# Optimization experiments

Measured on AMD Instinct MI355X. Metric: run time of the kernel, lower is better.

Reference implementation:

```python
import jax, jax.numpy as jnp
import numpy as np

H = W = 9
C = 16
D = 34
NHEAD = 2
HDIM = D // NHEAD  # 17
FF = 2048
NLAYERS = 2
EPS = 1e-5


def setup_inputs() -> dict:
    key = jax.random.key(0)
    ks = jax.random.split(key, 16)
    s = 0.05
    return {
        "obs": jax.random.normal(ks[0], (2, H, W), dtype=jnp.float32),
        "conv1_w": jax.random.normal(ks[1], (16, 2, 3, 3), dtype=jnp.float32) * s,
        "conv1_b": jnp.zeros((16,), jnp.float32),
        "conv2_w": jax.random.normal(ks[2], (16, 16, 3, 3), dtype=jnp.float32) * s,
        "conv2_b": jnp.zeros((16,), jnp.float32),
        "in_proj_w": jax.random.normal(ks[3], (NLAYERS, 3 * D, D), dtype=jnp.float32) * s,
        "in_proj_b": jnp.zeros((NLAYERS, 3 * D), jnp.float32),
        "out_proj_w": jax.random.normal(ks[4], (NLAYERS, D, D), dtype=jnp.float32) * s,
        "out_proj_b": jnp.zeros((NLAYERS, D), jnp.float32),
        "lin1_w": jax.random.normal(ks[5], (NLAYERS, FF, D), dtype=jnp.float32) * s,
        "lin1_b": jnp.zeros((NLAYERS, FF), jnp.float32),
        "lin2_w": jax.random.normal(ks[6], (NLAYERS, D, FF), dtype=jnp.float32) * s,
        "lin2_b": jnp.zeros((NLAYERS, D), jnp.float32),
        "ln1_g": jnp.ones((NLAYERS, D), jnp.float32),
        "ln1_b": jnp.zeros((NLAYERS, D), jnp.float32),
        "ln2_g": jnp.ones((NLAYERS, D), jnp.float32),
        "ln2_b": jnp.zeros((NLAYERS, D), jnp.float32),
    }


def _layer_norm(x, g, b):
    m = jnp.mean(x, axis=-1, keepdims=True)
    v = jnp.mean(jnp.square(x - m), axis=-1, keepdims=True)
    return (x - m) * jax.lax.rsqrt(v + EPS) * g + b


def _encoder_layer(x, ipw, ipb, opw, opb, l1w, l1b, l2w, l2b, g1, b1, g2, b2):
    # x: [S, D]. Post-norm TransformerEncoderLayer, eval mode (no dropout).
    S = x.shape[0]
    qkv = x @ ipw.T + ipb  # [S, 3D]
    q, k, v = jnp.split(qkv, 3, axis=-1)
    q = q.reshape(S, NHEAD, HDIM).transpose(1, 0, 2)  # [h, S, d]
    k = k.reshape(S, NHEAD, HDIM).transpose(1, 0, 2)
    v = v.reshape(S, NHEAD, HDIM).transpose(1, 0, 2)
    scores = jnp.einsum("hqd,hkd->hqk", q, k) / jnp.sqrt(jnp.float32(HDIM))
    attn = jax.nn.softmax(scores, axis=-1)
    o = jnp.einsum("hqk,hkd->hqd", attn, v)  # [h, S, d]
    o = o.transpose(1, 0, 2).reshape(S, D)
    o = o @ opw.T + opb
    x = _layer_norm(x + o, g1, b1)
    f = jax.nn.relu(x @ l1w.T + l1b) @ l2w.T + l2b
    return _layer_norm(x + f, g2, b2)


def _conv(x, w, b):
    y = jax.lax.conv_general_dilated(
        x, w, window_strides=(1, 1), padding="SAME",
        dimension_numbers=("NCHW", "OIHW", "NCHW"))
    return jax.nn.relu(y + b[None, :, None, None])


def reference(obs, conv1_w, conv1_b, conv2_w, conv2_b, in_proj_w, in_proj_b,
              out_proj_w, out_proj_b, lin1_w, lin1_b, lin2_w, lin2_b,
              ln1_g, ln1_b, ln2_g, ln2_b):
    x = obs[None]  # [1, 2, H, W]
    x = _conv(x, conv1_w, conv1_b)
    x = _conv(x, conv2_w, conv2_b)
    hw = H * W
    cell_emb = x[0].reshape(C, hw).T  # [hw, C]
    idx = jnp.arange(hw)
    r = (idx // W).astype(jnp.float32)
    c = (idx % W).astype(jnp.float32)
    dx = (r[:, None] - r[None, :]) / ((H - 1) / 2.0)  # [hw, hw]
    dy = (c[:, None] - c[None, :]) / ((W - 1) / 2.0)
    tok_i = jnp.broadcast_to(cell_emb[:, None, :], (hw, hw, C))
    tok_j = jnp.broadcast_to(cell_emb[None, :, :], (hw, hw, C))
    rel = jnp.stack([dx, dy], axis=-1)  # [hw, hw, 2]
    tokens = jnp.concatenate([tok_i, tok_j, rel], axis=-1).reshape(hw * hw, D)
    for l in range(NLAYERS):
        tokens = _encoder_layer(
            tokens, in_proj_w[l], in_proj_b[l], out_proj_w[l], out_proj_b[l],
            lin1_w[l], lin1_b[l], lin2_w[l], lin2_b[l],
            ln1_g[l], ln1_b[l], ln2_g[l], ln2_b[l])
    agent_idx = jnp.argmax(obs[0].reshape(-1))
    start = agent_idx * hw
    agent_tokens = jax.lax.dynamic_slice(tokens, (start, 0), (hw, D))
    return agent_tokens.mean(axis=0)  # [D]
```

## Files before the change

### kernel.cpp

```cpp
#include <hip/hip_runtime.h>
#include <hip/hip_bf16.h>

#define HH 9
#define WW 9
#define HW 81
#define CC 16
#define DD 34
#define SS 6561
#define NHEAD 2
#define HD 17
#define FF 2048
#define EPSF 1e-5f

#define NTILES 52
#define NSPLIT2 26
#define QB 64

#define NIP 7168
#define NOP 3072
#define NW1 131072
#define NW2 98304
#define NLTOT (NIP + NOP + NW1 + NW2)
#define LPREP_BLOCKS 1872
#define NKF 425984
#define NVF 212992
#define NV16 13312
#define ZERO_WORDS 332800
#define ZERO_BLOCKS 1300

typedef __attribute__((ext_vector_type(8))) short bf16x8;
typedef __attribute__((ext_vector_type(4))) float f32x4;

__device__ __forceinline__ unsigned short f2b(float f) {
  unsigned int u = __float_as_uint(f);
  u += 0x7fffu + ((u >> 16) & 1u);
  return (unsigned short)(u >> 16);
}

__global__ __launch_bounds__(256) void prep_kernel(
    const float* __restrict__ obs, const float* __restrict__ w1, const float* __restrict__ b1,
    const float* __restrict__ w2, const float* __restrict__ b2,
    float* __restrict__ cell, int* __restrict__ aidx,
    const float* __restrict__ ipw, const float* __restrict__ opw,
    const float* __restrict__ l1w, const float* __restrict__ l2w,
    unsigned short* __restrict__ ipwp, unsigned short* __restrict__ opwp,
    unsigned short* __restrict__ w1p, unsigned short* __restrict__ w2p,
    unsigned short* __restrict__ kfp, unsigned short* __restrict__ vfp,
    float* __restrict__ v16) {
  int bx = blockIdx.x;
  int t = threadIdx.x;
  if (bx == 0) {
    __shared__ float s_obs[2][11][11];
    __shared__ float s_w1[288];
    __shared__ float s_w2[2304];
    __shared__ float s_b1[16], s_b2[16];
    __shared__ float y1[CC][121];
    for (int i = t; i < 2 * 121; i += 256) ((float*)s_obs)[i] = 0.f;
    for (int i = t; i < CC * 121; i += 256) ((float*)y1)[i] = 0.f;
    for (int i = t; i < 288; i += 256) s_w1[i] = w1[i];
    for (int i = t; i < 2304; i += 256) s_w2[i] = w2[i];
    if (t < 16) { s_b1[t] = b1[t]; s_b2[t] = b2[t]; }
    __syncthreads();
    for (int i = t; i < 2 * HW; i += 256) {
      int ic = i / HW, p = i % HW;
      s_obs[ic][1 + p / WW][1 + p % WW] = obs[i];
    }
    __syncthreads();
    if (t == 0) {
      int best = 0; float bv = s_obs[0][1][1];
      for (int p = 1; p < HW; p++) {
        float v = s_obs[0][1 + p / WW][1 + p % WW];
        if (v > bv) { bv = v; best = p; }
      }
      *aidx = best;
    }
    for (int idx = t; idx < CC * HW; idx += 256) {
      int c = idx / HW, p = idx % HW;
      int i = p / WW, j = p % WW;
      float acc = s_b1[c];
#pragma unroll
      for (int ic = 0; ic < 2; ic++)
#pragma unroll
        for (int di = 0; di < 3; di++)
#pragma unroll
          for (int dj = 0; dj < 3; dj++)
            acc += s_obs[ic][i + di][j + dj] * s_w1[((c * 2 + ic) * 3 + di) * 3 + dj];
      y1[c][(i + 1) * 11 + (j + 1)] = fmaxf(acc, 0.f);
    }
    __syncthreads();
    for (int idx = t; idx < CC * HW; idx += 256) {
      int c = idx / HW, p = idx % HW;
      int i = p / WW, j = p % WW;
      float acc = s_b2[c];
#pragma unroll
      for (int ic = 0; ic < CC; ic++)
#pragma unroll
        for (int di = 0; di < 3; di++)
#pragma unroll
          for (int dj = 0; dj < 3; dj++)
            acc += y1[ic][(i + di) * 11 + (j + dj)] * s_w2[((c * CC + ic) * 3 + di) * 3 + dj];
      cell[p * CC + c] = fmaxf(acc, 0.f);
    }
  } else if (bx <= LPREP_BLOCKS) {
    int i = (bx - 1) * 256 + t;
    int layer = i / NLTOT;
    int r = i % NLTOT;
    if (r < NIP) {
      int n = r >> 6, k = r & 63;
      ipwp[layer * NIP + r] =
          (n < 102 && k < DD) ? f2b(ipw[(size_t)layer * 102 * DD + n * DD + k]) : (unsigned short)0;
    } else if (r < NIP + NOP) {
      int rr = r - NIP;
      int n = rr >> 6, k = rr & 63;
      opwp[layer * NOP + rr] =
          (n < DD && k < DD) ? f2b(opw[(size_t)layer * DD * DD + n * DD + k]) : (unsigned short)0;
    } else if (r < NIP + NOP + NW1) {
      int rr = r - NIP - NOP;
      int f = rr >> 6, k = rr & 63;
      w1p[layer * NW1 + rr] =
          (k < DD) ? f2b(l1w[(size_t)layer * FF * DD + f * DD + k]) : (unsigned short)0;
    } else {
      int rr = r - NIP - NOP - NW1;
      int d = rr >> 11, kk = rr & 2047;
      w2p[layer * NW2 + rr] =
          (d < DD) ? f2b(l2w[(size_t)layer * DD * FF + d * FF + kk]) : (unsigned short)0;
    }
  } else {
    int zi = (bx - 1 - LPREP_BLOCKS) * 256 + t;
    if (zi < NKF / 2) ((unsigned int*)kfp)[zi] = 0u;
    else if (zi < NKF / 2 + NVF / 2) ((unsigned int*)vfp)[zi - NKF / 2] = 0u;
    else if (zi < ZERO_WORDS) v16[zi - NKF / 2 - NVF / 2] = 0.f;
  }
}

__global__ __launch_bounds__(256) void ptprep_kernel(
    const float* __restrict__ cell, const float* __restrict__ ipw,
    const float* __restrict__ ipb, float* __restrict__ Pt) {
  int idx = blockIdx.x * 256 + threadIdx.x;
  if (idx >= 2 * HW * 102) return;
  int part = idx / (HW * 102);
  int rem = idx % (HW * 102);
  int a = rem / 102, n = rem % 102;
  float ra = (float)(a / WW) * 0.25f, ca = (float)(a % WW) * 0.25f;
  float acc;
  if (part == 0) {
    acc = ipb[n] + ipw[n * DD + 32] * ra + ipw[n * DD + 33] * ca;
    for (int f = 0; f < CC; f++) acc += ipw[n * DD + f] * cell[a * CC + f];
  } else {
    acc = -(ipw[n * DD + 32] * ra + ipw[n * DD + 33] * ca);
    for (int f = 0; f < CC; f++) acc += ipw[n * DD + CC + f] * cell[a * CC + f];
  }
  Pt[idx] = acc;
}

__global__ __launch_bounds__(256) void fl1_kernel(
    const float* __restrict__ cell, const float* __restrict__ Pt,
    const unsigned short* __restrict__ opwp, const float* __restrict__ opb,
    const float* __restrict__ g1v, const float* __restrict__ b1v,
    const unsigned short* __restrict__ w1p, const unsigned short* __restrict__ w2p,
    const float* __restrict__ fb1, const float* __restrict__ fb2,
    const float* __restrict__ g2v, const float* __restrict__ b2v,
    float* __restrict__ x) {
  __shared__ float sk[2][2][HW][20];
  __shared__ float sv[2][2][HW][20];
  __shared__ __align__(16) unsigned short soA[16 * 72];
  __shared__ float sxF[16][35];
  __shared__ __align__(16) unsigned short sxA2[16 * 72];
  __shared__ float sxF2[16][35];
  __shared__ __align__(16) unsigned short hw_[4][16 * 40];
  __shared__ float yred[4][16][49];
  int t = threadIdx.x;
  int w = t >> 6, lane = t & 63, quad = lane >> 4, col = lane & 15;
  int r0 = blockIdx.x * 16;
  int nr = min(16, SS - r0);

  for (int i = t; i < 16 * 72; i += 256) { soA[i] = 0; sxA2[i] = 0; }
  for (int i = t; i < 16 * 35; i += 256) { ((float*)sxF)[i] = 0.f; ((float*)sxF2)[i] = 0.f; }
  for (int i = t; i < 2 * 2 * HW * HD; i += 256) {
    int d = i % HD, a = (i / HD) % HW, part = (i / (HD * HW)) & 1, h = i / (HD * HW * 2);
    const float* base = Pt + (size_t)part * HW * 102 + a * 102;
    sk[h][part][a][d] = base[DD + h * HD + d];
    sv[h][part][a][d] = base[2 * DD + h * HD + d];
  }
  for (int i = t; i < nr * DD; i += 256) {
    int r = i / DD, d = i - r * DD;
    int row = r0 + r;
    int ii = row / HW, jj = row - ii * HW;
    float v;
    if (d < CC) v = cell[ii * CC + d];
    else if (d < 2 * CC) v = cell[jj * CC + (d - CC)];
    else if (d == 32) v = (float)((ii / WW) - (jj / WW)) * 0.25f;
    else v = (float)((ii % WW) - (jj % WW)) * 0.25f;
    sxF[r][d] = v;
  }
  __syncthreads();

  {
    int tl = t >> 4, sub = t & 15;
    int h = (sub >> 3) & 1, p = (sub >> 2) & 1, asp = sub & 3;
    int row = r0 + tl;
    int tc = row < SS ? row : SS - 1;
    int ii = tc / HW, jj = tc % HW;
    const float scale = 0.24253562503633297f;
    const float* p0 = Pt + ii * 102 + h * HD;
    const float* p1 = Pt + (size_t)HW * 102 + jj * 102 + h * HD;
    float q[HD];
#pragma unroll
    for (int d = 0; d < HD; d++) q[d] = (p0[d] + p1[d]) * scale;
    float S = 0.f, EV[HD];
#pragma unroll
    for (int d = 0; d < HD; d++) EV[d] = 0.f;
    for (int a = asp; a < HW; a += 4) {
      float s = 0.f;
#pragma unroll
      for (int d = 0; d < HD; d++) s += q[d] * sk[h][p][a][d];
      float e = __expf(fminf(s, 70.f));
      S += e;
#pragma unroll
      for (int d = 0; d < HD; d++) EV[d] += e * sv[h][p][a][d];
    }
    S += __shfl_xor(S, 1); S += __shfl_xor(S, 2);
#pragma unroll
    for (int d = 0; d < HD; d++) { EV[d] += __shfl_xor(EV[d], 1); EV[d] += __shfl_xor(EV[d], 2); }
    float So = __shfl_xor(S, 4);
    float EVo[HD];
#pragma unroll
    for (int d = 0; d < HD; d++) EVo[d] = __shfl_xor(EV[d], 4);
    float inv = 1.f / S, invo = 1.f / So;
    if ((sub & 7) == 0 && tl < nr) {
#pragma unroll
      for (int d = 0; d < HD; d++)
        soA[tl * 72 + h * HD + d] = f2b(EV[d] * inv + EVo[d] * invo);
    }
  }
  __syncthreads();

  if (w == 0) {
    bf16x8 a0 = *(const bf16x8*)&soA[col * 72 + quad * 8];
    bf16x8 a1 = *(const bf16x8*)&soA[col * 72 + 32 + quad * 8];
    f32x4 y[3];
#pragma unroll
    for (int nt = 0; nt < 3; nt++) {
      int n = nt * 16 + col;
      bf16x8 b0 = *(const bf16x8*)&opwp[n * 64 + quad * 8];
      bf16x8 b1 = *(const bf16x8*)&opwp[n * 64 + 32 + quad * 8];
      f32x4 acc = {0.f, 0.f, 0.f, 0.f};
      acc = __builtin_amdgcn_mfma_f32_16x16x32_bf16(a0, b0, acc, 0, 0, 0);
      y[nt] = __builtin_amdgcn_mfma_f32_16x16x32_bf16(a1, b1, acc, 0, 0, 0);
    }
    float yv[3][4];
    float s1[4] = {0.f, 0.f, 0.f, 0.f}, s2[4] = {0.f, 0.f, 0.f, 0.f};
#pragma unroll
    for (int nt = 0; nt < 3; nt++) {
      int d = nt * 16 + col;
      bool vd = d < DD;
      float ob = vd ? opb[d] : 0.f;
#pragma unroll
      for (int r = 0; r < 4; r++) {
        int row = quad * 4 + r;
        float v = vd ? (y[nt][r] + ob + sxF[row][d]) : 0.f;
        yv[nt][r] = v;
        s1[r] += v;
        s2[r] += v * v;
      }
    }
#pragma unroll
    for (int msk = 1; msk <= 8; msk <<= 1)
#pragma unroll
      for (int r = 0; r < 4; r++) {
        s1[r] += __shfl_xor(s1[r], msk);
        s2[r] += __shfl_xor(s2[r], msk);
      }
#pragma unroll
    for (int r = 0; r < 4; r++) {
      int row = quad * 4 + r;
      float mean = s1[r] * (1.f / DD);
      float var = s2[r] * (1.f / DD) - mean * mean;
      float rs = rsqrtf(var + EPSF);
#pragma unroll
      for (int nt = 0; nt < 3; nt++) {
        int d = nt * 16 + col;
        if (d < DD) {
          float o = (yv[nt][r] - mean) * rs * g1v[d] + b1v[d];
          sxF2[row][d] = o;
          sxA2[row * 72 + d] = f2b(o);
        }
      }
    }
  }
  __syncthreads();

  bf16x8 a0 = *(const bf16x8*)&sxA2[col * 72 + quad * 8];
  bf16x8 a1 = *(const bf16x8*)&sxA2[col * 72 + 32 + quad * 8];
  unsigned short* myh = &hw_[w][0];
  f32x4 acc3[3];
#pragma unroll
  for (int nt = 0; nt < 3; nt++) acc3[nt] = (f32x4){0.f, 0.f, 0.f, 0.f};
  for (int kt = 0; kt < 16; kt++) {
    int fbase = kt * 128 + w * 32;
#pragma unroll
    for (int nt = 0; nt < 2; nt++) {
      int f = fbase + nt * 16 + col;
      bf16x8 b0f = *(const bf16x8*)&w1p[f * 64 + quad * 8];
      bf16x8 b1f = *(const bf16x8*)&w1p[f * 64 + 32 + quad * 8];
      f32x4 hacc = {0.f, 0.f, 0.f, 0.f};
      hacc = __builtin_amdgcn_mfma_f32_16x16x32_bf16(a0, b0f, hacc, 0, 0, 0);
      hacc = __builtin_amdgcn_mfma_f32_16x16x32_bf16(a1, b1f, hacc, 0, 0, 0);
      float bias = fb1[f];
#pragma unroll
      for (int r = 0; r < 4; r++) {
        float hv = fmaxf(hacc[r] + bias, 0.f);
        myh[(quad * 4 + r) * 40 + nt * 16 + col] = f2b(hv);
      }
    }
    bf16x8 pa = *(const bf16x8*)&myh[col * 40 + quad * 8];
#pragma unroll
    for (int nt = 0; nt < 3; nt++) {
      int n = nt * 16 + col;
      bf16x8 wb = *(const bf16x8*)&w2p[(size_t)n * FF + fbase + quad * 8];
      acc3[nt] = __builtin_amdgcn_mfma_f32_16x16x32_bf16(pa, wb, acc3[nt], 0, 0, 0);
    }
  }
#pragma unroll
  for (int nt = 0; nt < 3; nt++)
#pragma unroll
    for (int r = 0; r < 4; r++)
      yred[w][quad * 4 + r][nt * 16 + col] = acc3[nt][r];
  __syncthreads();
  if (w == 0) {
    float yv[3][4];
    float s1[4] = {0.f, 0.f, 0.f, 0.f}, s2[4] = {0.f, 0.f, 0.f, 0.f};
#pragma unroll
    for (int nt = 0; nt < 3; nt++) {
      int d = nt * 16 + col;
      bool valid = d < DD;
      float b2x = valid ? fb2[d] : 0.f;
#pragma unroll
      for (int r = 0; r < 4; r++) {
        int row = quad * 4 + r;
        float v = yred[0][row][nt * 16 + col] + yred[1][row][nt * 16 + col]
                + yred[2][row][nt * 16 + col] + yred[3][row][nt * 16 + col];
        v = valid ? (v + b2x + sxF2[row][d]) : 0.f;
        yv[nt][r] = v;
        s1[r] += v;
        s2[r] += v * v;
      }
    }
#pragma unroll
    for (int msk = 1; msk <= 8; msk <<= 1)
#pragma unroll
      for (int r = 0; r < 4; r++) {
        s1[r] += __shfl_xor(s1[r], msk);
        s2[r] += __shfl_xor(s2[r], msk);
      }
#pragma unroll
    for (int r = 0; r < 4; r++) {
      int row = quad * 4 + r;
      if (row >= nr) continue;
      float mean = s1[r] * (1.f / DD);
      float var = s2[r] * (1.f / DD) - mean * mean;
      float rs = rsqrtf(var + EPSF);
#pragma unroll
      for (int nt = 0; nt < 3; nt++) {
        int d = nt * 16 + col;
        if (d < DD)
          x[(size_t)(r0 + row) * DD + d] = (yv[nt][r] - mean) * rs * g2v[d] + b2v[d];
      }
    }
  }
}

__global__ __launch_bounds__(256) void qkv2_kernel(
    const float* __restrict__ x, const unsigned short* __restrict__ ipwp,
    const float* __restrict__ ipb, const int* __restrict__ abase,
    float* __restrict__ qkv, unsigned short* __restrict__ kfp,
    unsigned short* __restrict__ vfp, float* __restrict__ v16) {
  __shared__ __align__(16) unsigned short sxA[32 * 72];
  int t = threadIdx.x;
  int w = t >> 6, lane = t & 63, quad = lane >> 4, col = lane & 15;
  int m0 = (w & 1) * 16, half = w >> 1;
  bool qpart = blockIdx.x >= 206;
  int row0 = qpart ? (abase[0] * HW + (blockIdx.x - 206) * 32) : blockIdx.x * 32;
  int nr = min(32, SS - row0);
  for (int i = t; i < 32 * 72; i += 256) sxA[i] = 0;
  __syncthreads();
  for (int i = t; i < nr * DD; i += 256) {
    int r = i / DD, d = i - r * DD;
    sxA[r * 72 + d] = f2b(x[(size_t)(row0 + r) * DD + d]);
  }
  __syncthreads();
  bf16x8 a0 = *(const bf16x8*)&sxA[(m0 + col) * 72 + quad * 8];
  bf16x8 a1 = *(const bf16x8*)&sxA[(m0 + col) * 72 + 32 + quad * 8];
  if (!qpart) {
    int ntc = half ? 2 : 3;
    for (int nt2 = 0; nt2 < ntc; nt2++) {
      int nt = half * 3 + nt2;
      int n = DD + nt * 16 + col;
      int nc = n < 112 ? n : 111;
      bf16x8 b0 = *(const bf16x8*)&ipwp[nc * 64 + quad * 8];
      bf16x8 b1 = *(const bf16x8*)&ipwp[nc * 64 + 32 + quad * 8];
      f32x4 acc = {0.f, 0.f, 0.f, 0.f};
      acc = __builtin_amdgcn_mfma_f32_16x16x32_bf16(a0, b0, acc, 0, 0, 0);
      acc = __builtin_amdgcn_mfma_f32_16x16x32_bf16(a1, b1, acc, 0, 0, 0);
      if (n < 102) {
        float bias = ipb[n];
        int kd = n - DD;
#pragma unroll
        for (int r = 0; r < 4; r++) {
          int m = m0 + quad * 4 + r;
          if (m >= nr) continue;
          int tok = row0 + m;
          float val = acc[r] + bias;
          int T = tok >> 7, tl = tok & 127;
          if (kd < 2 * HD) {
            int h = kd >= HD;
            int d = kd - h * HD;
            int colf = tl >> 3, ntk = tl & 7;
            kfp[(((size_t)h * NTILES + T) * 8 + ntk) * 512 +
                ((d >> 3) * 16 + colf) * 8 + (d & 7)] = f2b(val);
          } else {
            int vd = kd - 2 * HD;
            int h = vd >= HD;
            int d = vd - h * HD;
            if (d < 16) {
              int c = tl >> 5, qf = (tl >> 3) & 3, j = tl & 7;
              vfp[(((size_t)h * NTILES + T) * 4 + c) * 512 +
                  (qf * 16 + d) * 8 + j] = f2b(val);
            } else {
              v16[(size_t)h * (NTILES * 128) + tok] = val;
            }
          }
        }
      }
    }
  } else {
    int ntc = half ? 1 : 2;
    for (int nt2 = 0; nt2 < ntc; nt2++) {
      int nt = half * 2 + nt2;
      int n = nt * 16 + col;
      bf16x8 b0 = *(const bf16x8*)&ipwp[n * 64 + quad * 8];
      bf16x8 b1 = *(const bf16x8*)&ipwp[n * 64 + 32 + quad * 8];
      f32x4 acc = {0.f, 0.f, 0.f, 0.f};
      acc = __builtin_amdgcn_mfma_f32_16x16x32_bf16(a0, b0, acc, 0, 0, 0);
      acc = __builtin_amdgcn_mfma_f32_16x16x32_bf16(a1, b1, acc, 0, 0, 0);
      if (n < DD) {
        float bias = ipb[n];
#pragma unroll
        for (int r = 0; r < 4; r++) {
          int m = row0 + m0 + quad * 4 + r;
          if (m < SS) qkv[(size_t)m * 102 + n] = acc[r] + bias;
        }
      }
    }
  }
}

__global__ __launch_bounds__(256) void attn2_kernel(
    const float* __restrict__ qkv, const unsigned short* __restrict__ kfp,
    const unsigned short* __restrict__ vfp, const float* __restrict__ v16,
    const int* __restrict__ abase,
    float* __restrict__ opart, float* __restrict__ lpart) {
  __shared__ __align__(16) unsigned short scb[4][16 * 136];
  int t = threadIdx.x, w = t >> 6, lane = t & 63, quad = lane >> 4, col = lane & 15;
  int h = blockIdx.y, sp = blockIdx.z;
  int base = abase[0] * HW;
  int q0 = blockIdx.x * QB;
  const float scale = 0.24253562503633297f;
  const unsigned short* kf = kfp + (size_t)h * (NTILES * 8 * 512);
  const unsigned short* vf = vfp + (size_t)h * (NTILES * 4 * 512);
  const float* v16h = v16 + (size_t)h * (NTILES * 128);
  unsigned short* myscb = &scb[w][0];

  int mq = base + q0 + w * 16 + col;
  int qc = mq < SS ? mq : SS - 1;
  bf16x8 aq;
#pragma unroll
  for (int j = 0; j < 8; j++) {
    int d = quad * 8 + j;
    aq[j] = (short)((d < HD) ? f2b(qkv[(size_t)qc * 102 + h * HD + d] * scale) : 0);
  }

  f32x4 oacc = {0.f, 0.f, 0.f, 0.f};
  float o16a[4] = {0.f, 0.f, 0.f, 0.f};
  float lreg[4] = {0.f, 0.f, 0.f, 0.f};

  for (int tile = sp; tile < NTILES; tile += NSPLIT2) {
    int k0 = tile * 128;
    const unsigned short* kt = kf + (size_t)tile * (8 * 512);
    f32x4 s[8];
#pragma unroll
    for (int nt = 0; nt < 8; nt++) {
      bf16x8 kb = *(const bf16x8*)(kt + nt * 512 + lane * 8);
      f32x4 z = {0.f, 0.f, 0.f, 0.f};
      s[nt] = __builtin_amdgcn_mfma_f32_16x16x32_bf16(aq, kb, z, 0, 0, 0);
    }
    if (k0 + 128 > SS) {
#pragma unroll
      for (int nt = 0; nt < 8; nt++)
        if (k0 + col * 8 + nt >= SS) {
          s[nt][0] = -1e30f; s[nt][1] = -1e30f; s[nt][2] = -1e30f; s[nt][3] = -1e30f;
        }
    }
#pragma unroll
    for (int r = 0; r < 4; r++) {
      bf16x8 pv;
      float psl = 0.f;
#pragma unroll
      for (int nt = 0; nt < 8; nt++) {
        float p = __expf(fminf(s[nt][r], 70.f));
        s[nt][r] = p;
        psl += p;
        pv[nt] = (short)f2b(p);
      }
      lreg[r] += psl;
      *(bf16x8*)(myscb + (quad * 4 + r) * 136 + col * 8) = pv;
    }
    f32x4 va = *(const f32x4*)(v16h + k0 + col * 8);
    f32x4 vb4 = *(const f32x4*)(v16h + k0 + col * 8 + 4);
#pragma unroll
    for (int r = 0; r < 4; r++) {
      o16a[r] += s[0][r] * va[0] + s[1][r] * va[1] + s[2][r] * va[2] + s[3][r] * va[3]
               + s[4][r] * vb4[0] + s[5][r] * vb4[1] + s[6][r] * vb4[2] + s[7][r] * vb4[3];
    }
    const unsigned short* vt = vf + (size_t)tile * (4 * 512);
#pragma unroll
    for (int c = 0; c < 4; c++) {
      bf16x8 pa = *(const bf16x8*)(myscb + col * 136 + c * 32 + quad * 8);
      bf16x8 vbf = *(const bf16x8*)(vt + c * 512 + lane * 8);
      oacc = __builtin_amdgcn_mfma_f32_16x16x32_bf16(pa, vbf, oacc, 0, 0, 0);
    }
  }
#pragma unroll
  for (int msk = 1; msk <= 8; msk <<= 1)
#pragma unroll
    for (int r = 0; r < 4; r++) {
      o16a[r] += __shfl_xor(o16a[r], msk);
      lreg[r] += __shfl_xor(lreg[r], msk);
    }
  size_t obase = ((size_t)sp * NHEAD + h) * 128;
#pragma unroll
  for (int r = 0; r < 4; r++) {
    int ql = q0 + w * 16 + quad * 4 + r;
    if (ql < HW) {
      opart[(obase + ql) * HD + col] = oacc[r];
      if (col == 0) {
        opart[(obase + ql) * HD + 16] = o16a[r];
        lpart[obase + ql] = lreg[r];
      }
    }
  }
}

__global__ __launch_bounds__(256) void fl2_kernel(
    const float* __restrict__ opart, const float* __restrict__ lpart,
    const unsigned short* __restrict__ opwp, const float* __restrict__ opb,
    const float* __restrict__ g1v, const float* __restrict__ b1v,
    const unsigned short* __restrict__ w1p, const unsigned short* __restrict__ w2p,
    const float* __restrict__ fb1, const float* __restrict__ fb2,
    const float* __restrict__ g2v, const float* __restrict__ b2v,
    const int* __restrict__ abase, float* __restrict__ x) {
  __shared__ __align__(16) unsigned short soA[16 * 72];
  __shared__ float sxF[16][35];
  __shared__ __align__(16) unsigned short sxA2[16 * 72];
  __shared__ float sxF2[16][35];
  __shared__ __align__(16) unsigned short hw_[4][16 * 40];
  __shared__ float yred[4][16][49];
  int t = threadIdx.x;
  int w = t >> 6, lane = t & 63, quad = lane >> 4, col = lane & 15;
  int base = abase[0] * HW;
  int ql0 = blockIdx.x * 16;
  int nr = min(16, HW - ql0);
  int r0 = base + ql0;

  for (int i = t; i < 16 * 72; i += 256) { soA[i] = 0; sxA2[i] = 0; }
  for (int i = t; i < 16 * 35; i += 256) { ((float*)sxF)[i] = 0.f; ((float*)sxF2)[i] = 0.f; }
  __syncthreads();
  for (int i = t; i < nr * DD; i += 256) {
    int r = i / DD, rem = i - r * DD;
    sxF[r][rem] = x[(size_t)(r0 + r) * DD + rem];
    int ql = ql0 + r;
    int h = rem / HD, d = rem - h * HD;
    float L = 0.f, O = 0.f;
#pragma unroll
    for (int s = 0; s < NSPLIT2; s++) {
      L += lpart[((size_t)s * NHEAD + h) * 128 + ql];
      O += opart[(((size_t)s * NHEAD + h) * 128 + ql) * HD + d];
    }
    soA[r * 72 + rem] = f2b(O / L);
  }
  __syncthreads();
  if (w == 0) {
    bf16x8 a0 = *(const bf16x8*)&soA[col * 72 + quad * 8];
    bf16x8 a1 = *(const bf16x8*)&soA[col * 72 + 32 + quad * 8];
    f32x4 y[3];
#pragma unroll
    for (int nt = 0; nt < 3; nt++) {
      int n = nt * 16 + col;
      bf16x8 b0 = *(const bf16x8*)&opwp[n * 64 + quad * 8];
      bf16x8 b1 = *(const bf16x8*)&opwp[n * 64 + 32 + quad * 8];
      f32x4 acc = {0.f, 0.f, 0.f, 0.f};
      acc = __builtin_amdgcn_mfma_f32_16x16x32_bf16(a0, b0, acc, 0, 0, 0);
      y[nt] = __builtin_amdgcn_mfma_f32_16x16x32_bf16(a1, b1, acc, 0, 0, 0);
    }
    float yv[3][4];
    float s1[4] = {0.f, 0.f, 0.f, 0.f}, s2[4] = {0.f, 0.f, 0.f, 0.f};
#pragma unroll
    for (int nt = 0; nt < 3; nt++) {
      int d = nt * 16 + col;
      bool vd = d < DD;
      float ob = vd ? opb[d] : 0.f;
#pragma unroll
      for (int r = 0; r < 4; r++) {
        int row = quad * 4 + r;
        float v = vd ? (y[nt][r] + ob + sxF[row][d]) : 0.f;
        yv[nt][r] = v;
        s1[r] += v;
        s2[r] += v * v;
      }
    }
#pragma unroll
    for (int msk = 1; msk <= 8; msk <<= 1)
#pragma unroll
      for (int r = 0; r < 4; r++) {
        s1[r] += __shfl_xor(s1[r], msk);
        s2[r] += __shfl_xor(s2[r], msk);
      }
#pragma unroll
    for (int r = 0; r < 4; r++) {
      int row = quad * 4 + r;
      float mean = s1[r] * (1.f / DD);
      float var = s2[r] * (1.f / DD) - mean * mean;
      float rs = rsqrtf(var + EPSF);
#pragma unroll
      for (int nt = 0; nt < 3; nt++) {
        int d = nt * 16 + col;
        if (d < DD) {
          float o = (yv[nt][r] - mean) * rs * g1v[d] + b1v[d];
          sxF2[row][d] = o;
          sxA2[row * 72 + d] = f2b(o);
        }
      }
    }
  }
  __syncthreads();
  bf16x8 a0 = *(const bf16x8*)&sxA2[col * 72 + quad * 8];
  bf16x8 a1 = *(const bf16x8*)&sxA2[col * 72 + 32 + quad * 8];
  unsigned short* myh = &hw_[w][0];
  f32x4 acc3[3];
#pragma unroll
  for (int nt = 0; nt < 3; nt++) acc3[nt] = (f32x4){0.f, 0.f, 0.f, 0.f};
  for (int kt = 0; kt < 16; kt++) {
    int fbase = kt * 128 + w * 32;
#pragma unroll
    for (int nt = 0; nt < 2; nt++) {
      int f = fbase + nt * 16 + col;
      bf16x8 b0f = *(const bf16x8*)&w1p[f * 64 + quad * 8];
      bf16x8 b1f = *(const bf16x8*)&w1p[f * 64 + 32 + quad * 8];
      f32x4 hacc = {0.f, 0.f, 0.f, 0.f};
      hacc = __builtin_amdgcn_mfma_f32_16x16x32_bf16(a0, b0f, hacc, 0, 0, 0);
      hacc = __builtin_amdgcn_mfma_f32_16x16x32_bf16(a1, b1f, hacc, 0, 0, 0);
      float bias = fb1[f];
#pragma unroll
      for (int r = 0; r < 4; r++) {
        float hv = fmaxf(hacc[r] + bias, 0.f);
        myh[(quad * 4 + r) * 40 + nt * 16 + col] = f2b(hv);
      }
    }
    bf16x8 pa = *(const bf16x8*)&myh[col * 40 + quad * 8];
#pragma unroll
    for (int nt = 0; nt < 3; nt++) {
      int n = nt * 16 + col;
      bf16x8 wb = *(const bf16x8*)&w2p[(size_t)n * FF + fbase + quad * 8];
      acc3[nt] = __builtin_amdgcn_mfma_f32_16x16x32_bf16(pa, wb, acc3[nt], 0, 0, 0);
    }
  }
#pragma unroll
  for (int nt = 0; nt < 3; nt++)
#pragma unroll
    for (int r = 0; r < 4; r++)
      yred[w][quad * 4 + r][nt * 16 + col] = acc3[nt][r];
  __syncthreads();
  if (w == 0) {
    float yv[3][4];
    float s1[4] = {0.f, 0.f, 0.f, 0.f}, s2[4] = {0.f, 0.f, 0.f, 0.f};
#pragma unroll
    for (int nt = 0; nt < 3; nt++) {
      int d = nt * 16 + col;
      bool valid = d < DD;
      float b2x = valid ? fb2[d] : 0.f;
#pragma unroll
      for (int r = 0; r < 4; r++) {
        int row = quad * 4 + r;
        float v = yred[0][row][nt * 16 + col] + yred[1][row][nt * 16 + col]
                + yred[2][row][nt * 16 + col] + yred[3][row][nt * 16 + col];
        v = valid ? (v + b2x + sxF2[row][d]) : 0.f;
        yv[nt][r] = v;
        s1[r] += v;
        s2[r] += v * v;
      }
    }
#pragma unroll
    for (int msk = 1; msk <= 8; msk <<= 1)
#pragma unroll
      for (int r = 0; r < 4; r++) {
        s1[r] += __shfl_xor(s1[r], msk);
        s2[r] += __shfl_xor(s2[r], msk);
      }
#pragma unroll
    for (int r = 0; r < 4; r++) {
      int row = quad * 4 + r;
      if (row >= nr) continue;
      float mean = s1[r] * (1.f / DD);
      float var = s2[r] * (1.f / DD) - mean * mean;
      float rs = rsqrtf(var + EPSF);
#pragma unroll
      for (int nt = 0; nt < 3; nt++) {
        int d = nt * 16 + col;
        if (d < DD)
          x[(size_t)(r0 + row) * DD + d] = (yv[nt][r] - mean) * rs * g2v[d] + b2v[d];
      }
    }
  }
}

__global__ __launch_bounds__(64) void final_kernel(
    const float* __restrict__ x, const int* __restrict__ aidx, float* __restrict__ out) {
  int d = threadIdx.x;
  if (d >= DD) return;
  int start = (*aidx) * HW;
  float acc = 0.f;
  for (int j = 0; j < HW; j++) acc += x[(size_t)(start + j) * DD + d];
  out[d] = acc * (1.f / HW);
}

extern "C" void kernel_launch(void* const* d_in, const int* in_sizes, int n_in,
                              void* d_out, int out_size, void* d_ws, size_t ws_size,
                              hipStream_t stream) {
  const float* obs = (const float*)d_in[0];
  const float* c1w = (const float*)d_in[1];
  const float* c1b = (const float*)d_in[2];
  const float* c2w = (const float*)d_in[3];
  const float* c2b = (const float*)d_in[4];
  const float* ipw = (const float*)d_in[5];
  const float* ipb = (const float*)d_in[6];
  const float* opw = (const float*)d_in[7];
  const float* opb = (const float*)d_in[8];
  const float* l1w = (const float*)d_in[9];
  const float* l1b = (const float*)d_in[10];
  const float* l2w = (const float*)d_in[11];
  const float* l2b = (const float*)d_in[12];
  const float* g1 = (const float*)d_in[13];
  const float* b1 = (const float*)d_in[14];
  const float* g2 = (const float*)d_in[15];
  const float* b2 = (const float*)d_in[16];
  float* out = (float*)d_out;

  float* ws = (float*)d_ws;
  size_t off = 0;
  float* x     = ws + off; off += SS * DD;
  float* qkv   = ws + off; off += SS * 102;
  float* cell  = ws + off; off += HW * CC;
  int*   aidx  = (int*)(ws + off); off += 1;
  off = (off + 3) & ~(size_t)3;
  float* Pt    = ws + off; off += 2 * HW * 102;
  float* opart = ws + off; off += (size_t)NSPLIT2 * NHEAD * 128 * HD;
  float* lpart = ws + off; off += (size_t)NSPLIT2 * NHEAD * 128;
  off = (off + 3) & ~(size_t)3;
  unsigned short* kfp  = (unsigned short*)(ws + off); off += NKF / 2;
  unsigned short* vfp  = (unsigned short*)(ws + off); off += NVF / 2;
  float* v16 = ws + off; off += NV16;
  unsigned short* ipwp = (unsigned short*)(ws + off); off += 2 * NIP / 2;
  unsigned short* opwp = (unsigned short*)(ws + off); off += 2 * NOP / 2;
  unsigned short* w1p  = (unsigned short*)(ws + off); off += 2 * NW1 / 2;
  unsigned short* w2p  = (unsigned short*)(ws + off); off += 2 * NW2 / 2;

  const int prep_grid = 1 + LPREP_BLOCKS + ZERO_BLOCKS;
  const int pt_blocks = (2 * HW * 102 + 255) / 256;
  const int fl1_blocks = (SS + 15) / 16;

  prep_kernel<<<prep_grid, 256, 0, stream>>>(
      obs, c1w, c1b, c2w, c2b, cell, aidx,
      ipw, opw, l1w, l2w, ipwp, opwp, w1p, w2p, kfp, vfp, v16);
  ptprep_kernel<<<pt_blocks, 256, 0, stream>>>(cell, ipw, ipb, Pt);
  fl1_kernel<<<fl1_blocks, 256, 0, stream>>>(
      cell, Pt, opwp, opb, g1, b1, w1p, w2p, l1b, l2b, g2, b2, x);
  qkv2_kernel<<<210, 256, 0, stream>>>(
      x, ipwp + NIP, ipb + 102, aidx, qkv, kfp, vfp, v16);
  dim3 a2g(2, NHEAD, NSPLIT2);
  attn2_kernel<<<a2g, 256, 0, stream>>>(qkv, kfp, vfp, v16, aidx, opart, lpart);
  fl2_kernel<<<6, 256, 0, stream>>>(
      opart, lpart, opwp + NOP, opb + DD, g1 + DD, b1 + DD,
      w1p + NW1, w2p + NW2, l1b + FF, l2b + DD, g2 + DD, b2 + DD, aidx, x);
  final_kernel<<<1, 64, 0, stream>>>(x, aidx, out);
}
```

Baseline: 203.2 us.

## Factor layer-1 attention exponentials into precomputed tables and use MFMA for PV

Layer-1 queries are the sum of a term that depends on i and a term that depends on j. Likewise the keys split into two halves. So exp(q·k) factors into a product of two exponentials, each indexed by (row, key). A new expprep kernel precomputes these exponential tables and a bf16 V fragment that carries a row of ones to yield the softmax denominator. fl1 now multiplies the two tables, writes the weights as bf16 to LDS and does P·V with MFMA. This replaces per-row scalar dot products and exps, at the cost of an extra kernel launch, extra global reads, bf16 rounding of the attention weights, and the exponent clamp moving from 70 to 40.

Result: faster. 195.5 us (-3.8%).

```diff
diff --git a/kernel.cpp b/kernel.cpp
--- a/kernel.cpp
+++ b/kernel.cpp
@@ -27,6 +27,9 @@
 #define NV16 13312
 #define ZERO_WORDS 332800
 #define ZERO_BLOCKS 1300
+
+#define NEAB 124416
+#define NVFL1 12288
 
 typedef __attribute__((ext_vector_type(8))) short bf16x8;
 typedef __attribute__((ext_vector_type(4))) float f32x4;
@@ -153,16 +156,49 @@
   Pt[idx] = acc;
 }
 
+__global__ __launch_bounds__(256) void expprep_kernel(
+    const float* __restrict__ Pt, float* __restrict__ eAB,
+    unsigned short* __restrict__ vfragL1) {
+  int idx = blockIdx.x * 256 + threadIdx.x;
+  const float scale = 0.24253562503633297f;
+  if (idx < NEAB) {
+    int a = idx % 96; int rest = idx / 96;
+    int row = rest % 81; rest /= 81;
+    int ab = rest & 1, p = (rest >> 1) & 1, h = rest >> 2;
+    float e = 0.f;
+    if (a < HW) {
+      const float* qrow = Pt + (size_t)ab * (HW * 102) + row * 102 + h * HD;
+      const float* krow = Pt + (size_t)p * (HW * 102) + a * 102 + DD + h * HD;
+      float dot = 0.f;
+#pragma unroll
+      for (int d = 0; d < HD; d++) dot += qrow[d] * krow[d];
+      e = __expf(fminf(dot * scale, 40.f));
+    }
+    eAB[idx] = e;
+  } else if (idx < NEAB + NVFL1) {
+    int j = idx - NEAB;
+    int a = j % 96; int rest = j / 96;
+    int n = rest % 32; rest /= 32;
+    int p = rest & 1, h = rest >> 1;
+    float v = 0.f;
+    if (a < HW) {
+      if (n < HD) v = Pt[(size_t)p * (HW * 102) + a * 102 + 2 * DD + h * HD + n];
+      else if (n == HD) v = 1.f;
+    }
+    vfragL1[((size_t)(h * 2 + p) * 32 + n) * 96 + a] = f2b(v);
+  }
+}
+
 __global__ __launch_bounds__(256) void fl1_kernel(
-    const float* __restrict__ cell, const float* __restrict__ Pt,
+    const float* __restrict__ cell, const float* __restrict__ eAB,
+    const unsigned short* __restrict__ vfragL1,
     const unsigned short* __restrict__ opwp, const float* __restrict__ opb,
     const float* __restrict__ g1v, const float* __restrict__ b1v,
     const unsigned short* __restrict__ w1p, const unsigned short* __restrict__ w2p,
     const float* __restrict__ fb1, const float* __restrict__ fb2,
     const float* __restrict__ g2v, const float* __restrict__ b2v,
     float* __restrict__ x) {
-  __shared__ float sk[2][2][HW][20];
-  __shared__ float sv[2][2][HW][20];
+  __shared__ __align__(16) unsigned short sE[4][16 * 96];
   __shared__ __align__(16) unsigned short soA[16 * 72];
   __shared__ float sxF[16][35];
   __shared__ __align__(16) unsigned short sxA2[16 * 72];
@@ -176,12 +212,6 @@
 
   for (int i = t; i < 16 * 72; i += 256) { soA[i] = 0; sxA2[i] = 0; }
   for (int i = t; i < 16 * 35; i += 256) { ((float*)sxF)[i] = 0.f; ((float*)sxF2)[i] = 0.f; }
-  for (int i = t; i < 2 * 2 * HW * HD; i += 256) {
-    int d = i % HD, a = (i / HD) % HW, part = (i / (HD * HW)) & 1, h = i / (HD * HW * 2);
-    const float* base = Pt + (size_t)part * HW * 102 + a * 102;
-    sk[h][part][a][d] = base[DD + h * HD + d];
-    sv[h][part][a][d] = base[2 * DD + h * HD + d];
-  }
   for (int i = t; i < nr * DD; i += 256) {
     int r = i / DD, d = i - r * DD;
     int row = r0 + r;
@@ -193,45 +223,50 @@
     else v = (float)((ii % WW) - (jj % WW)) * 0.25f;
     sxF[r][d] = v;
   }
-  __syncthreads();
 
   {
-    int tl = t >> 4, sub = t & 15;
-    int h = (sub >> 3) & 1, p = (sub >> 2) & 1, asp = sub & 3;
+    int h = w >> 1, p = w & 1;
+    const float* eA = eAB + ((size_t)((h * 2 + p) * 2 + 0) * 81) * 96;
+    const float* eB = eAB + ((size_t)((h * 2 + p) * 2 + 1) * 81) * 96;
+    int tl = lane >> 2, asub = lane & 3;
     int row = r0 + tl;
     int tc = row < SS ? row : SS - 1;
-    int ii = tc / HW, jj = tc % HW;
-    const float scale = 0.24253562503633297f;
-    const float* p0 = Pt + ii * 102 + h * HD;
-    const float* p1 = Pt + (size_t)HW * 102 + jj * 102 + h * HD;
-    float q[HD];
-#pragma unroll
-    for (int d = 0; d < HD; d++) q[d] = (p0[d] + p1[d]) * scale;
-    float S = 0.f, EV[HD];
-#pragma unroll
-    for (int d = 0; d < HD; d++) EV[d] = 0.f;
-    for (int a = asp; a < HW; a += 4) {
-      float s = 0.f;
-#pragma unroll
-      for (int d = 0; d < HD; d++) s += q[d] * sk[h][p][a][d];
-      float e = __expf(fminf(s, 70.f));
-      S += e;
-#pragma unroll
-      for (int d = 0; d < HD; d++) EV[d] += e * sv[h][p][a][d];
-    }
-    S += __shfl_xor(S, 1); S += __shfl_xor(S, 2);
-#pragma unroll
-    for (int d = 0; d < HD; d++) { EV[d] += __shfl_xor(EV[d], 1); EV[d] += __shfl_xor(EV[d], 2); }
-    float So = __shfl_xor(S, 4);
-    float EVo[HD];
-#pragma unroll
-    for (int d = 0; d < HD; d++) EVo[d] = __shfl_xor(EV[d], 4);
-    float inv = 1.f / S, invo = 1.f / So;
-    if ((sub & 7) == 0 && tl < nr) {
-#pragma unroll
-      for (int d = 0; d < HD; d++)
-        soA[tl * 72 + h * HD + d] = f2b(EV[d] * inv + EVo[d] * invo);
-    }
+    int it = tc / HW, jt = tc - it * HW;
+    const float* eAr = eA + it * 96 + asub * 24;
+    const float* eBr = eB + jt * 96 + asub * 24;
+    unsigned short etmp[24];
+#pragma unroll
+    for (int k = 0; k < 24; k++) etmp[k] = f2b(eAr[k] * eBr[k]);
+    unsigned short* Eb = &sE[w][tl * 96 + asub * 24];
+#pragma unroll
+    for (int k = 0; k < 3; k++)
+      *(bf16x8*)(Eb + k * 8) = *(bf16x8*)(etmp + k * 8);
+    const unsigned short* vf = vfragL1 + (size_t)(h * 2 + p) * 32 * 96;
+    f32x4 acc0 = {0.f, 0.f, 0.f, 0.f}, acc1 = {0.f, 0.f, 0.f, 0.f};
+#pragma unroll
+    for (int c = 0; c < 3; c++) {
+      bf16x8 ea = *(const bf16x8*)&sE[w][col * 96 + c * 32 + quad * 8];
+      bf16x8 vb0 = *(const bf16x8*)&vf[col * 96 + c * 32 + quad * 8];
+      bf16x8 vb1 = *(const bf16x8*)&vf[(16 + col) * 96 + c * 32 + quad * 8];
+      acc0 = __builtin_amdgcn_mfma_f32_16x16x32_bf16(ea, vb0, acc0, 0, 0, 0);
+      acc1 = __builtin_amdgcn_mfma_f32_16x16x32_bf16(ea, vb1, acc1, 0, 0, 0);
+    }
+    float Sr[4];
+#pragma unroll
+    for (int r = 0; r < 4; r++) Sr[r] = __shfl(acc1[r], (lane & 48) + 1);
+#pragma unroll
+    for (int r = 0; r < 4; r++) {
+      int rr = quad * 4 + r;
+      float inv = 1.f / Sr[r];
+      yred[w][rr][col] = acc0[r] * inv;
+      if (col == 0) yred[w][rr][16] = acc1[r] * inv;
+    }
+  }
+  __syncthreads();
+  for (int i = t; i < 16 * DD; i += 256) {
+    int r = i / DD, dd = i - r * DD;
+    int h2 = dd / HD, d2 = dd - h2 * HD;
+    soA[r * 72 + dd] = f2b(yred[2 * h2][r][d2] + yred[2 * h2 + 1][r][d2]);
   }
   __syncthreads();
 
@@ -765,7 +800,9 @@
   float* Pt    = ws + off; off += 2 * HW * 102;
   float* opart = ws + off; off += (size_t)NSPLIT2 * NHEAD * 128 * HD;
   float* lpart = ws + off; off += (size_t)NSPLIT2 * NHEAD * 128;
+  float* eAB   = ws + off; off += NEAB;
   off = (off + 3) & ~(size_t)3;
+  unsigned short* vfragL1 = (unsigned short*)(ws + off); off += NVFL1 / 2;
   unsigned short* kfp  = (unsigned short*)(ws + off); off += NKF / 2;
   unsigned short* vfp  = (unsigned short*)(ws + off); off += NVF / 2;
   float* v16 = ws + off; off += NV16;
@@ -776,14 +813,16 @@
 
   const int prep_grid = 1 + LPREP_BLOCKS + ZERO_BLOCKS;
   const int pt_blocks = (2 * HW * 102 + 255) / 256;
+  const int exp_blocks = (NEAB + NVFL1 + 255) / 256;
   const int fl1_blocks = (SS + 15) / 16;
 
   prep_kernel<<<prep_grid, 256, 0, stream>>>(
       obs, c1w, c1b, c2w, c2b, cell, aidx,
       ipw, opw, l1w, l2w, ipwp, opwp, w1p, w2p, kfp, vfp, v16);
   ptprep_kernel<<<pt_blocks, 256, 0, stream>>>(cell, ipw, ipb, Pt);
+  expprep_kernel<<<exp_blocks, 256, 0, stream>>>(Pt, eAB, vfragL1);
   fl1_kernel<<<fl1_blocks, 256, 0, stream>>>(
-      cell, Pt, opwp, opb, g1, b1, w1p, w2p, l1b, l2b, g2, b2, x);
+      cell, eAB, vfragL1, opwp, opb, g1, b1, w1p, w2p, l1b, l2b, g2, b2, x);
   qkv2_kernel<<<210, 256, 0, stream>>>(
       x, ipwp + NIP, ipb + 102, aidx, qkv, kfp, vfp, v16);
   dim3 a2g(2, NHEAD, NSPLIT2);
```
